# Optimization experiments

Hardware: AMD Instinct MI355X
Metric: run time of the kernel (lower is better)

Reference implementation:

```python
import jax, jax.numpy as jnp
import numpy as np

N = 16384; T = 65536; H = 128; G = 512; E = 65536; NEI = 32768
NIT = 4  # num_interactions
NL = 4   # finaldepth (hidden layers after the first)
EPS = 1e-5
INV = float(1.0 / np.sqrt(1.0 + EPS))  # fresh BatchNorm1d in eval mode: running_mean=0, running_var=1


def _bn(x, g, b):
    # eval-mode BatchNorm with mean=0, var=1: (x - 0)/sqrt(1+eps)*gamma + beta
    return x * (g * INV) + b


def setup_inputs() -> dict:
    key = jax.random.key(0)
    ks = jax.random.split(key, 16)
    inp = {}
    inp["node_positions"] = jax.random.normal(ks[0], (N, 2), jnp.float32)
    inp["edge_index_2rd"] = jax.random.randint(ks[1], (3, T), 0, N)  # (i, j, k) triplets
    inp["edx_jk"] = jax.random.randint(ks[2], (T,), 0, E)
    inp["edx_ij"] = jax.random.randint(ks[3], (T,), 0, E)
    inp["num_edge_inside"] = NEI
    inp["node_to_feature"] = jax.random.randint(ks[4], (N,), 0, G)
    # mlp_geo: Linear(3, H) + BN
    inp["Wg"] = jax.random.normal(ks[5], (3, H), jnp.float32) / np.sqrt(3.0)
    inp["bg"] = jnp.zeros((H,), jnp.float32)
    inp["gamg"] = 1.0 + 0.1 * jax.random.normal(ks[6], (H,), jnp.float32)
    inp["betg"] = 0.1 * jax.random.normal(ks[7], (H,), jnp.float32)
    # per-interaction (NIT), per-edge-type-group (4) MLPs
    inp["W0"] = jax.random.normal(ks[8], (NIT, 4, 4 * H, H), jnp.float32) / np.sqrt(4.0 * H)
    inp["b0"] = jnp.zeros((NIT, 4, H), jnp.float32)
    inp["g0"] = 1.0 + 0.1 * jax.random.normal(ks[9], (NIT, 4, H), jnp.float32)
    inp["be0"] = 0.1 * jax.random.normal(ks[10], (NIT, 4, H), jnp.float32)
    inp["Wh"] = jax.random.normal(ks[11], (NIT, NL, 4, H, H), jnp.float32) / np.sqrt(float(H))
    inp["bh"] = jnp.zeros((NIT, NL, 4, H), jnp.float32)
    inp["gh"] = 1.0 + 0.1 * jax.random.normal(ks[12], (NIT, NL, 4, H), jnp.float32)
    inp["beh"] = 0.1 * jax.random.normal(ks[13], (NIT, NL, 4, H), jnp.float32)
    inp["att"] = jnp.ones((4,), jnp.float32)
    return inp


def reference(node_positions, Wg, bg, gamg, betg, W0, b0, g0, be0, Wh, bh, gh, beh, att,
              edge_index_2rd, edx_jk, edx_ij, num_edge_inside, node_to_feature):
    i, j, k = edge_index_2rd[0], edge_index_2rd[1], edge_index_2rd[2]
    # geometric features of each triplet (i<-j<-k)
    v1 = node_positions[j] - node_positions[i]   # [T,2]
    v2 = node_positions[k] - node_positions[j]   # [T,2]
    d_ij = jnp.linalg.norm(v1, axis=1)
    d_jk = jnp.linalg.norm(v2, axis=1)
    cross = v1[:, 0] * v2[:, 1] - v1[:, 1] * v2[:, 0]
    dot = jnp.sum(v1 * v2, axis=1)
    theta = jnp.arctan2(jnp.abs(cross), dot)
    geo = jnp.stack([d_ij, d_jk, theta], axis=-1)        # [T,3]
    geo = jax.nn.relu(_bn(geo @ Wg + bg, gamg, betg))    # [T,H] geo_encoding

    # 4 mutually exclusive edge-type masks
    in1 = edx_ij < num_edge_inside
    in2 = edx_jk < num_edge_inside
    masks = jnp.stack([in1 & in2, in1 & ~in2, ~in1 & in2, ~in1 & ~in2], axis=0)  # [4,T]
    mask_f = masks.astype(geo.dtype)[:, :, None]         # [4,T,1]

    num_nodes = node_positions.shape[0]
    nf = jnp.zeros((num_nodes, H), geo.dtype)            # input_feature = zeros
    outs = []
    for it in range(NIT):
        x = jnp.concatenate([nf[i], nf[j], nf[k], geo], axis=-1)  # [T,4H]
        h = jnp.einsum('ti,gio->gto', x, W0[it]) + b0[it][:, None, :]
        h = jax.nn.relu(_bn(h, g0[it][:, None, :], be0[it][:, None, :]))
        for l in range(NL):
            h = jnp.einsum('gti,gio->gto', h, Wh[it, l]) + bh[it, l][:, None, :]
            h = jax.nn.relu(_bn(h, gh[it, l][:, None, :], beh[it, l][:, None, :]))
        h = jax.nn.leaky_relu(h, 0.01) * att[:, None, None]       # [4,T,H]
        x_out = jnp.sum(h * mask_f, axis=0)                       # disjoint masks -> select
        nf = jax.ops.segment_sum(x_out, i, num_segments=num_nodes)  # scatter_add over i
        outs.append(nf)
    out = jnp.concatenate(outs, axis=1)                           # [N, NIT*H]
    emb = jax.ops.segment_sum(out, node_to_feature, num_segments=G)  # global_add_pool
    return jnp.minimum(emb, 1.0e6)
```

## Files before the change

### kernel.cpp

```cpp
#include <hip/hip_runtime.h>
#include <hip/hip_bf16.h>
#include <math.h>

#define N_NODES 16384
#define T_TRI   65536
#define H_DIM   128
#define G_POOL  512
#define NITER   4
#define NLAY    4
#define RMAX    (T_TRI + 512)
#define MT64    (RMAX / 64)

#define INV_STD 0.9999950000374996f

typedef __attribute__((ext_vector_type(8))) short bhalf8;
typedef __attribute__((ext_vector_type(4))) float f32x4;

__device__ __forceinline__ unsigned short f2b(float f) {
    unsigned int u = __float_as_uint(f);
    unsigned int r = (u + 0x7fffu + ((u >> 16) & 1u)) >> 16;
    return (unsigned short)r;
}
__device__ __forceinline__ float b2f(unsigned short b) {
    return __uint_as_float(((unsigned int)b) << 16);
}


__device__ __forceinline__ int group_of(int eij, int ejk, int nei) {
    return ((eij < nei) ? 0 : 2) + ((ejk < nei) ? 0 : 1);
}

__global__ void histboth_k(const int* __restrict__ edxjk, const int* __restrict__ edxij,
                           const int* __restrict__ neip, const int* __restrict__ eidx,
                           int* __restrict__ ints, int* __restrict__ cnt) {
    __shared__ int lc[4];
    if (threadIdx.x < 4) lc[threadIdx.x] = 0;
    __syncthreads();
    int t = blockIdx.x * 256 + threadIdx.x;
    int nei = *neip;
    int g = group_of(edxij[t], edxjk[t], nei);
    atomicAdd(&lc[g], 1);
    atomicAdd(&cnt[eidx[t]], 1);
    __syncthreads();
    if (threadIdx.x < 4) atomicAdd(&ints[threadIdx.x], lc[threadIdx.x]);
}

__global__ void scanoff_k(int* __restrict__ ints, int* __restrict__ cnt,
                          int* __restrict__ row_start) {
    __shared__ int part[256];
    int tid = threadIdx.x;
    if (tid == 0) {
        int a = 0;
        ints[8] = 0;
        for (int g = 0; g < 4; ++g) {
            a = (a + ints[g] + 127) & ~127;
            ints[9 + g] = a;
        }
    }
    int base = tid * 64;
    int s = 0;
    for (int q = 0; q < 64; ++q) s += cnt[base + q];
    part[tid] = s;
    __syncthreads();
    if (tid == 0) {
        int run = 0;
        for (int q = 0; q < 256; ++q) { int v = part[q]; part[q] = run; run += v; }
        row_start[N_NODES] = run;
    }
    __syncthreads();
    int p = part[tid];
    for (int q = 0; q < 64; ++q) {
        int c = cnt[base + q];
        row_start[base + q] = p;
        cnt[base + q] = p;
        p += c;
    }
}

__global__ void scatboth_k(const int* __restrict__ edxjk, const int* __restrict__ edxij,
                           const int* __restrict__ neip, const int* __restrict__ eidx,
                           int* __restrict__ ints, int* __restrict__ rowmap,
                           int* __restrict__ cursor, int* __restrict__ row_ids) {
    int t = blockIdx.x * 256 + threadIdx.x;
    int nei = *neip;
    int g = group_of(edxij[t], edxjk[t], nei);
    int lane = threadIdx.x & 63;
    unsigned long long msame = 0;
    #pragma unroll
    for (int q = 0; q < 4; ++q) {
        unsigned long long mq = __ballot(g == q);
        if (g == q) msame = mq;
    }
    int leader = __ffsll((long long)msame) - 1;
    int rank = __popcll(msame & ((1ull << lane) - 1ull));
    int base = 0;
    if (lane == leader) base = atomicAdd(&ints[4 + g], __popcll(msame));
    base = __shfl(base, leader);
    int pos = ints[8 + g] + base + rank;
    rowmap[pos] = t;
    int slot = atomicAdd(&cursor[eidx[t]], 1);
    row_ids[slot] = pos;
}


__global__ void t0_k(const float* __restrict__ W0, unsigned short* __restrict__ WT0) {
    __shared__ float t[32][33];
    int b = blockIdx.x;
    int ig = b >> 6;
    int kt = (b >> 2) & 15;
    int nt = b & 3;
    int tx = threadIdx.x & 31, ty = threadIdx.x >> 5;
    const float* src = W0 + ((size_t)ig * 512 + kt * 32) * 128 + nt * 32;
    #pragma unroll
    for (int q = 0; q < 4; ++q) { int r = q * 8 + ty; t[r][tx] = src[(size_t)r * 128 + tx]; }
    __syncthreads();
    unsigned short* dst = WT0 + ((size_t)ig * 128 + nt * 32) * 512 + kt * 32;
    #pragma unroll
    for (int q = 0; q < 4; ++q) { int r = q * 8 + ty; dst[(size_t)r * 512 + tx] = f2b(t[tx][r]); }
}

__global__ void th_k(const float* __restrict__ Wh, unsigned short* __restrict__ WTh) {
    __shared__ float t[32][33];
    int b = blockIdx.x;
    int ilg = b >> 4;
    int kt = (b >> 2) & 3;
    int nt = b & 3;
    int tx = threadIdx.x & 31, ty = threadIdx.x >> 5;
    const float* src = Wh + ((size_t)ilg * 128 + kt * 32) * 128 + nt * 32;
    #pragma unroll
    for (int q = 0; q < 4; ++q) { int r = q * 8 + ty; t[r][tx] = src[(size_t)r * 128 + tx]; }
    __syncthreads();
    unsigned short* dst = WTh + ((size_t)ilg * 128 + nt * 32) * 128 + kt * 32;
    #pragma unroll
    for (int q = 0; q < 4; ++q) { int r = q * 8 + ty; dst[(size_t)r * 128 + tx] = f2b(t[tx][r]); }
}


__global__ void geo_k(const float* __restrict__ pos, const int* __restrict__ eidx,
                      const float* __restrict__ Wg, const float* __restrict__ bg,
                      const float* __restrict__ gamg, const float* __restrict__ betg,
                      unsigned short* __restrict__ geob) {
    int t = blockIdx.x * 16 + (threadIdx.x >> 4);
    int h0 = (threadIdx.x & 15) * 8;
    int ni = eidx[t], nj = eidx[T_TRI + t], nk = eidx[2 * T_TRI + t];
    float ix = pos[2 * ni], iy = pos[2 * ni + 1];
    float jx = pos[2 * nj], jy = pos[2 * nj + 1];
    float kx = pos[2 * nk], ky = pos[2 * nk + 1];
    float v1x = jx - ix, v1y = jy - iy;
    float v2x = kx - jx, v2y = ky - jy;
    float dij = sqrtf(v1x * v1x + v1y * v1y);
    float djk = sqrtf(v2x * v2x + v2y * v2y);
    float cr = v1x * v2y - v1y * v2x;
    float dt = v1x * v2x + v1y * v2y;
    float th = atan2f(fabsf(cr), dt);
    unsigned int ov[4];
    #pragma unroll
    for (int q = 0; q < 4; ++q) {
        unsigned int lo = 0, hi = 0;
        #pragma unroll
        for (int e = 0; e < 2; ++e) {
            int h = h0 + q * 2 + e;
            float v = dij * Wg[h] + djk * Wg[128 + h] + th * Wg[256 + h] + bg[h];
            v = v * (gamg[h] * INV_STD) + betg[h];
            v = fmaxf(v, 0.0f);
            if (e == 0) lo = f2b(v); else hi = f2b(v);
        }
        ov[q] = lo | (hi << 16);
    }
    int4 o = { (int)ov[0], (int)ov[1], (int)ov[2], (int)ov[3] };
    *reinterpret_cast<int4*>(&geob[(size_t)t * 128 + h0]) = o;
}


template<int SKIPNF>
__global__ __launch_bounds__(256, 4) void chain_k(
    const unsigned short* __restrict__ nfb, const unsigned short* __restrict__ geob,
    const int* __restrict__ eidx, const int* __restrict__ rowmap,
    const int* __restrict__ aoff, const unsigned short* __restrict__ WT0,
    const float* __restrict__ b0, const float* __restrict__ g0, const float* __restrict__ be0,
    const unsigned short* __restrict__ WTh,
    const float* __restrict__ bhp, const float* __restrict__ ghp, const float* __restrict__ behp,
    const float* __restrict__ att, unsigned short* __restrict__ hfinal,
    int it) {
    __shared__ unsigned short sh[64 * 128];
    __shared__ unsigned short sa[2][64 * 64];

    const int r0 = blockIdx.x * 64;
    int g = 0;
    if (r0 >= aoff[1]) g = 1;
    if (r0 >= aoff[2]) g = 2;
    if (r0 >= aoff[3]) g = 3;
    const int tid = threadIdx.x;
    const int lane = tid & 63;
    const int w = tid >> 6;
    const int lr = lane & 15, lq = lane >> 4;

    const int myrow = tid >> 3;
    const int mycolb = (tid & 7) * 8;
    int ttv[2], offi[2], offj[2], offk2[2], offt[2];
    #pragma unroll
    for (int p = 0; p < 2; ++p) {
        int row = p * 32 + myrow;
        int tt = rowmap[r0 + row];
        ttv[p] = tt;
        int ts = tt < 0 ? 0 : tt;
        offt[p] = ts * 128;
        if (!SKIPNF) {
            offi[p]  = eidx[ts] * 128;
            offj[p]  = eidx[T_TRI + ts] * 128;
            offk2[p] = eidx[2 * T_TRI + ts] * 128;
        }
    }

    f32x4 acc[4][2];
    const f32x4 zero4 = {0.f, 0.f, 0.f, 0.f};
    #pragma unroll
    for (int m = 0; m < 4; ++m)
        #pragma unroll
        for (int n = 0; n < 2; ++n) acc[m][n] = zero4;

    const unsigned short* Wt = WT0 + (size_t)(it * 4 + g) * 128 * 512;
    constexpr int KSTEPS = SKIPNF ? 2 : 8;
    constexpr int KBASE  = SKIPNF ? 384 : 0;
    int4 ra[2];

    {
        const int k0 = KBASE;
        const int region = k0 >> 7, half = k0 & 127;
        #pragma unroll
        for (int p = 0; p < 2; ++p) {
            int4 v = {0, 0, 0, 0};
            if (ttv[p] >= 0) {
                const unsigned short* src =
                    region == 0 ? nfb + offi[p] :
                    region == 1 ? nfb + offj[p] :
                    region == 2 ? nfb + offk2[p] :
                                  geob + offt[p];
                v = *reinterpret_cast<const int4*>(src + half + mycolb);
            }
            int row = p * 32 + myrow;
            *reinterpret_cast<int4*>(&sa[0][row * 64 + (((tid & 7) ^ (row & 7)) << 3)]) = v;
        }
        __syncthreads();
    }

    #pragma unroll
    for (int s = 0; s < KSTEPS; ++s) {
        const int cur = s & 1;
        const int k0 = KBASE + s * 64;
        if (s + 1 < KSTEPS) {
            const int k1 = k0 + 64;
            const int region = k1 >> 7, half = k1 & 127;
            #pragma unroll
            for (int p = 0; p < 2; ++p) {
                int4 v = {0, 0, 0, 0};
                if (ttv[p] >= 0) {
                    const unsigned short* src =
                        region == 0 ? nfb + offi[p] :
                        region == 1 ? nfb + offj[p] :
                        region == 2 ? nfb + offk2[p] :
                                      geob + offt[p];
                    v = *reinterpret_cast<const int4*>(src + half + mycolb);
                }
                ra[p] = v;
            }
        }
        bhalf8 rbf[2][2];
        #pragma unroll
        for (int n = 0; n < 2; ++n) {
            int nn = 32 * w + 16 * n + lr;
            #pragma unroll
            for (int ks = 0; ks < 2; ++ks)
                rbf[n][ks] = *reinterpret_cast<const bhalf8*>(Wt + (size_t)nn * 512 + k0 + ks * 32 + lq * 8);
        }
        #pragma unroll
        for (int ks = 0; ks < 2; ++ks) {
            bhalf8 af[4];
            #pragma unroll
            for (int m = 0; m < 4; ++m) {
                int row = 16 * m + lr;
                int c8 = (4 * ks + lq) ^ (row & 7);
                af[m] = *reinterpret_cast<const bhalf8*>(&sa[cur][row * 64 + (c8 << 3)]);
            }
            #pragma unroll
            for (int m = 0; m < 4; ++m)
                #pragma unroll
                for (int n = 0; n < 2; ++n)
                    acc[m][n] = __builtin_amdgcn_mfma_f32_16x16x32_bf16(af[m], rbf[n][ks], acc[m][n], 0, 0, 0);
        }
        if (s + 1 < KSTEPS) {
            #pragma unroll
            for (int p = 0; p < 2; ++p) {
                int row = p * 32 + myrow;
                *reinterpret_cast<int4*>(&sa[cur ^ 1][row * 64 + (((tid & 7) ^ (row & 7)) << 3)]) = ra[p];
            }
        }
        __syncthreads();
    }

    {
        const float* bb = b0 + (it * 4 + g) * 128;
        const float* gg = g0 + (it * 4 + g) * 128;
        const float* be = be0 + (it * 4 + g) * 128;
        #pragma unroll
        for (int n = 0; n < 2; ++n) {
            int col = 32 * w + 16 * n + lr;
            float sc = gg[col] * INV_STD;
            float bbc = bb[col], bec = be[col];
            int gc = col >> 3, cl = col & 7;
            #pragma unroll
            for (int m = 0; m < 4; ++m)
                #pragma unroll
                for (int r = 0; r < 4; ++r) {
                    int row = 16 * m + 4 * lq + r;
                    float v = fmaxf((acc[m][n][r] + bbc) * sc + bec, 0.0f);
                    sh[row * 128 + ((gc ^ (row & 7)) << 3) + cl] = f2b(v);
                }
        }
    }
    __syncthreads();

    for (int l = 0; l < NLAY; ++l) {
        const unsigned short* Wl = WTh + (size_t)((it * NLAY + l) * 4 + g) * 128 * 128;
        #pragma unroll
        for (int m = 0; m < 4; ++m)
            #pragma unroll
            for (int n = 0; n < 2; ++n) acc[m][n] = zero4;
        #pragma unroll
        for (int kk = 0; kk < 4; ++kk) {
            bhalf8 af[4], bf[2];
            #pragma unroll
            for (int n = 0; n < 2; ++n) {
                int nn = 32 * w + 16 * n + lr;
                bf[n] = *reinterpret_cast<const bhalf8*>(Wl + (size_t)nn * 128 + kk * 32 + lq * 8);
            }
            #pragma unroll
            for (int m = 0; m < 4; ++m) {
                int row = 16 * m + lr;
                int gc = (4 * kk + lq) ^ (row & 7);
                af[m] = *reinterpret_cast<const bhalf8*>(&sh[row * 128 + (gc << 3)]);
            }
            #pragma unroll
            for (int m = 0; m < 4; ++m)
                #pragma unroll
                for (int n = 0; n < 2; ++n)
                    acc[m][n] = __builtin_amdgcn_mfma_f32_16x16x32_bf16(af[m], bf[n], acc[m][n], 0, 0, 0);
        }
        __syncthreads();
        if (l + 1 < NLAY) {
            const int ilg = (it * NLAY + l) * 4 + g;
            const float* bb = bhp + (size_t)ilg * 128;
            const float* gg = ghp + (size_t)ilg * 128;
            const float* be = behp + (size_t)ilg * 128;
            #pragma unroll
            for (int n = 0; n < 2; ++n) {
                int col = 32 * w + 16 * n + lr;
                float sc = gg[col] * INV_STD;
                float bbc = bb[col], bec = be[col];
                int gc = col >> 3, cl = col & 7;
                #pragma unroll
                for (int m = 0; m < 4; ++m)
                    #pragma unroll
                    for (int r = 0; r < 4; ++r) {
                        int row = 16 * m + 4 * lq + r;
                        float v = fmaxf((acc[m][n][r] + bbc) * sc + bec, 0.0f);
                        sh[row * 128 + ((gc ^ (row & 7)) << 3) + cl] = f2b(v);
                    }
            }
            __syncthreads();
        }
    }

    {
        const int ilg = (it * NLAY + (NLAY - 1)) * 4 + g;
        const float* bb = bhp + (size_t)ilg * 128;
        const float* gg = ghp + (size_t)ilg * 128;
        const float* be = behp + (size_t)ilg * 128;
        float attg = att[g];
        #pragma unroll
        for (int n = 0; n < 2; ++n) {
            int col = 32 * w + 16 * n + lr;
            float sc = gg[col] * INV_STD;
            float bbc = bb[col], bec = be[col];
            int gc = col >> 3, cl = col & 7;
            #pragma unroll
            for (int m = 0; m < 4; ++m)
                #pragma unroll
                for (int r = 0; r < 4; ++r) {
                    int row = 16 * m + 4 * lq + r;
                    float v = fmaxf((acc[m][n][r] + bbc) * sc + bec, 0.0f) * attg;
                    sh[row * 128 + ((gc ^ (row & 7)) << 3) + cl] = f2b(v);
                }
        }
    }
    __syncthreads();
    #pragma unroll
    for (int p = 0; p < 4; ++p) {
        int idx = p * 256 + tid;
        int row = idx >> 4, gd = idx & 15;
        int4 v = *reinterpret_cast<const int4*>(&sh[row * 128 + ((gd ^ (row & 7)) << 3)]);
        *reinterpret_cast<int4*>(&hfinal[(size_t)(r0 + row) * 128 + gd * 8]) = v;
    }
}


__global__ void reduce_k(const unsigned short* __restrict__ hfinal,
                         const int* __restrict__ row_start, const int* __restrict__ row_ids,
                         const int* __restrict__ ntf, unsigned short* __restrict__ nfb,
                         float* __restrict__ emb, int itoff) {
    int n = blockIdx.x * 2 + (threadIdx.x >> 7);
    int c = threadIdx.x & 127;
    int s = row_start[n], e = row_start[n + 1];
    float acc = 0.0f;
    for (int r = s; r < e; ++r) {
        int rid = row_ids[r];
        acc += b2f(hfinal[(size_t)rid * 128 + c]);
    }
    nfb[(size_t)n * 128 + c] = f2b(acc);
    atomicAdd(&emb[(size_t)ntf[n] * 512 + itoff + c], acc);
}

__global__ void clamp_k(const float* __restrict__ emb, float* __restrict__ out) {
    int i = blockIdx.x * 256 + threadIdx.x;
    out[i] = fminf(emb[i], 1.0e6f);
}


extern "C" void kernel_launch(void* const* d_in, const int* in_sizes, int n_in,
                              void* d_out, int out_size, void* d_ws, size_t ws_size,
                              hipStream_t stream) {
    (void)in_sizes; (void)n_in; (void)out_size; (void)ws_size;
    const float* pos   = (const float*)d_in[0];
    const int*   eidx  = (const int*)d_in[1];
    const int*   edxjk = (const int*)d_in[2];
    const int*   edxij = (const int*)d_in[3];
    const int*   neip  = (const int*)d_in[4];
    const int*   ntf   = (const int*)d_in[5];
    const float* Wg    = (const float*)d_in[6];
    const float* bg    = (const float*)d_in[7];
    const float* gamg  = (const float*)d_in[8];
    const float* betg  = (const float*)d_in[9];
    const float* W0    = (const float*)d_in[10];
    const float* b0    = (const float*)d_in[11];
    const float* g0    = (const float*)d_in[12];
    const float* be0   = (const float*)d_in[13];
    const float* Wh    = (const float*)d_in[14];
    const float* bhp   = (const float*)d_in[15];
    const float* ghp   = (const float*)d_in[16];
    const float* behp  = (const float*)d_in[17];
    const float* att   = (const float*)d_in[18];

    char* w = (char*)d_ws;
    size_t off = 0;
    auto alloc = [&](size_t b) -> char* {
        char* p = w + off;
        off += (b + 255) & ~(size_t)255;
        return p;
    };
    int* ints            = (int*)alloc(256);
    int* rowmap          = (int*)alloc((size_t)RMAX * 4);
    int* cnt             = (int*)alloc((size_t)N_NODES * 4);
    int* row_start       = (int*)alloc((size_t)(N_NODES + 1) * 4);
    int* row_ids         = (int*)alloc((size_t)T_TRI * 4);
    unsigned short* WT0  = (unsigned short*)alloc((size_t)16 * 128 * 512 * 2);
    unsigned short* WTh  = (unsigned short*)alloc((size_t)64 * 128 * 128 * 2);
    unsigned short* geob = (unsigned short*)alloc((size_t)T_TRI * 128 * 2);
    unsigned short* nfb  = (unsigned short*)alloc((size_t)N_NODES * 128 * 2);
    unsigned short* hfin = (unsigned short*)alloc((size_t)RMAX * 128 * 2);
    float* emb           = (float*)alloc((size_t)G_POOL * 512 * 4);

    hipMemsetAsync(ints, 0, 256, stream);
    hipMemsetAsync(rowmap, 0xFF, (size_t)RMAX * 4, stream);
    hipMemsetAsync(cnt, 0, (size_t)N_NODES * 4, stream);
    hipMemsetAsync(emb, 0, (size_t)G_POOL * 512 * 4, stream);

    histboth_k<<<256, 256, 0, stream>>>(edxjk, edxij, neip, eidx, ints, cnt);
    scanoff_k<<<1, 256, 0, stream>>>(ints, cnt, row_start);
    scatboth_k<<<256, 256, 0, stream>>>(edxjk, edxij, neip, eidx, ints, rowmap, cnt, row_ids);
    t0_k<<<1024, 256, 0, stream>>>(W0, WT0);
    th_k<<<1024, 256, 0, stream>>>(Wh, WTh);
    geo_k<<<T_TRI / 16, 256, 0, stream>>>(pos, eidx, Wg, bg, gamg, betg, geob);

    for (int it = 0; it < NITER; ++it) {
        if (it == 0)
            chain_k<1><<<MT64, 256, 0, stream>>>(nfb, geob, eidx, rowmap, ints + 8, WT0, b0, g0, be0,
                                                 WTh, bhp, ghp, behp, att, hfin, it);
        else
            chain_k<0><<<MT64, 256, 0, stream>>>(nfb, geob, eidx, rowmap, ints + 8, WT0, b0, g0, be0,
                                                 WTh, bhp, ghp, behp, att, hfin, it);
        reduce_k<<<N_NODES / 2, 256, 0, stream>>>(hfin, row_start, row_ids, ntf, nfb, emb, it * 128);
    }

    clamp_k<<<1024, 256, 0, stream>>>(emb, (float*)d_out);
}
```

Measured before the change: 445.2 us.

## Restructure chain kernel to single-wave 32-row tiles with register-prefetched A

The MLP chain kernel moves from 256-thread blocks over 64 rows to one-wave blocks over 32 rows, each wave computing all 128 output columns. The first-layer A operand is gathered straight into registers with a 4-deep prefetch instead of being staged through double-buffered shared memory. The aim is to drop all __syncthreads and LDS staging while doubling the grid for occupancy. In exchange, each wave reloads the full weight matrices from global or cache for only 32 rows, and the larger accumulator set raises register pressure.

```diff
diff --git a/kernel.cpp b/kernel.cpp
--- a/kernel.cpp
+++ b/kernel.cpp
@@ -9,7 +9,7 @@
 #define NITER   4
 #define NLAY    4
 #define RMAX    (T_TRI + 512)
-#define MT64    (RMAX / 64)
+#define MT32    (RMAX / 32)
 
 #define INV_STD 0.9999950000374996f
 
@@ -173,7 +173,7 @@
 
 
 template<int SKIPNF>
-__global__ __launch_bounds__(256, 4) void chain_k(
+__global__ __launch_bounds__(64) void chain_k(
     const unsigned short* __restrict__ nfb, const unsigned short* __restrict__ geob,
     const int* __restrict__ eidx, const int* __restrict__ rowmap,
     const int* __restrict__ aoff, const unsigned short* __restrict__ WT0,
@@ -182,120 +182,78 @@
     const float* __restrict__ bhp, const float* __restrict__ ghp, const float* __restrict__ behp,
     const float* __restrict__ att, unsigned short* __restrict__ hfinal,
     int it) {
-    __shared__ unsigned short sh[64 * 128];
-    __shared__ unsigned short sa[2][64 * 64];
-
-    const int r0 = blockIdx.x * 64;
+    __shared__ unsigned short shw[32 * 128];
+
+    const int r0 = blockIdx.x * 32;
     int g = 0;
     if (r0 >= aoff[1]) g = 1;
     if (r0 >= aoff[2]) g = 2;
     if (r0 >= aoff[3]) g = 3;
-    const int tid = threadIdx.x;
-    const int lane = tid & 63;
-    const int w = tid >> 6;
+    const int lane = threadIdx.x & 63;
     const int lr = lane & 15, lq = lane >> 4;
 
-    const int myrow = tid >> 3;
-    const int mycolb = (tid & 7) * 8;
-    int ttv[2], offi[2], offj[2], offk2[2], offt[2];
-    #pragma unroll
-    for (int p = 0; p < 2; ++p) {
-        int row = p * 32 + myrow;
-        int tt = rowmap[r0 + row];
-        ttv[p] = tt;
+    int ttm[2];
+    const unsigned short* pi[2];
+    const unsigned short* pj[2];
+    const unsigned short* pk[2];
+    const unsigned short* pg[2];
+    #pragma unroll
+    for (int m = 0; m < 2; ++m) {
+        int tt = rowmap[r0 + 16 * m + lr];
+        ttm[m] = tt;
         int ts = tt < 0 ? 0 : tt;
-        offt[p] = ts * 128;
+        pg[m] = geob + (size_t)ts * 128;
         if (!SKIPNF) {
-            offi[p]  = eidx[ts] * 128;
-            offj[p]  = eidx[T_TRI + ts] * 128;
-            offk2[p] = eidx[2 * T_TRI + ts] * 128;
-        }
-    }
-
-    f32x4 acc[4][2];
+            pi[m] = nfb + (size_t)eidx[ts] * 128;
+            pj[m] = nfb + (size_t)eidx[T_TRI + ts] * 128;
+            pk[m] = nfb + (size_t)eidx[2 * T_TRI + ts] * 128;
+        } else {
+            pi[m] = pj[m] = pk[m] = pg[m];
+        }
+    }
+
+    f32x4 acc[2][8];
     const f32x4 zero4 = {0.f, 0.f, 0.f, 0.f};
     #pragma unroll
-    for (int m = 0; m < 4; ++m)
-        #pragma unroll
-        for (int n = 0; n < 2; ++n) acc[m][n] = zero4;
+    for (int m = 0; m < 2; ++m)
+        #pragma unroll
+        for (int n = 0; n < 8; ++n) acc[m][n] = zero4;
 
     const unsigned short* Wt = WT0 + (size_t)(it * 4 + g) * 128 * 512;
-    constexpr int KSTEPS = SKIPNF ? 2 : 8;
-    constexpr int KBASE  = SKIPNF ? 384 : 0;
-    int4 ra[2];
-
-    {
-        const int k0 = KBASE;
-        const int region = k0 >> 7, half = k0 & 127;
-        #pragma unroll
-        for (int p = 0; p < 2; ++p) {
-            int4 v = {0, 0, 0, 0};
-            if (ttv[p] >= 0) {
-                const unsigned short* src =
-                    region == 0 ? nfb + offi[p] :
-                    region == 1 ? nfb + offj[p] :
-                    region == 2 ? nfb + offk2[p] :
-                                  geob + offt[p];
-                v = *reinterpret_cast<const int4*>(src + half + mycolb);
-            }
-            int row = p * 32 + myrow;
-            *reinterpret_cast<int4*>(&sa[0][row * 64 + (((tid & 7) ^ (row & 7)) << 3)]) = v;
-        }
-        __syncthreads();
-    }
-
-    #pragma unroll
-    for (int s = 0; s < KSTEPS; ++s) {
-        const int cur = s & 1;
-        const int k0 = KBASE + s * 64;
-        if (s + 1 < KSTEPS) {
-            const int k1 = k0 + 64;
-            const int region = k1 >> 7, half = k1 & 127;
-            #pragma unroll
-            for (int p = 0; p < 2; ++p) {
-                int4 v = {0, 0, 0, 0};
-                if (ttv[p] >= 0) {
-                    const unsigned short* src =
-                        region == 0 ? nfb + offi[p] :
-                        region == 1 ? nfb + offj[p] :
-                        region == 2 ? nfb + offk2[p] :
-                                      geob + offt[p];
-                    v = *reinterpret_cast<const int4*>(src + half + mycolb);
-                }
-                ra[p] = v;
-            }
-        }
-        bhalf8 rbf[2][2];
-        #pragma unroll
-        for (int n = 0; n < 2; ++n) {
-            int nn = 32 * w + 16 * n + lr;
-            #pragma unroll
-            for (int ks = 0; ks < 2; ++ks)
-                rbf[n][ks] = *reinterpret_cast<const bhalf8*>(Wt + (size_t)nn * 512 + k0 + ks * 32 + lq * 8);
-        }
-        #pragma unroll
-        for (int ks = 0; ks < 2; ++ks) {
-            bhalf8 af[4];
-            #pragma unroll
-            for (int m = 0; m < 4; ++m) {
-                int row = 16 * m + lr;
-                int c8 = (4 * ks + lq) ^ (row & 7);
-                af[m] = *reinterpret_cast<const bhalf8*>(&sa[cur][row * 64 + (c8 << 3)]);
-            }
-            #pragma unroll
-            for (int m = 0; m < 4; ++m)
-                #pragma unroll
-                for (int n = 0; n < 2; ++n)
-                    acc[m][n] = __builtin_amdgcn_mfma_f32_16x16x32_bf16(af[m], rbf[n][ks], acc[m][n], 0, 0, 0);
-        }
-        if (s + 1 < KSTEPS) {
-            #pragma unroll
-            for (int p = 0; p < 2; ++p) {
-                int row = p * 32 + myrow;
-                *reinterpret_cast<int4*>(&sa[cur ^ 1][row * 64 + (((tid & 7) ^ (row & 7)) << 3)]) = ra[p];
-            }
-        }
-        __syncthreads();
+    constexpr int KS0 = SKIPNF ? 12 : 0;
+
+    auto loadA = [&](int ks, int m) -> int4 {
+        const int region = ks >> 2;
+        const int off = (ks & 3) * 32 + lq * 8;
+        const unsigned short* src =
+            region == 0 ? pi[m] : region == 1 ? pj[m] : region == 2 ? pk[m] : pg[m];
+        int4 v = {0, 0, 0, 0};
+        if (ttm[m] >= 0) v = *reinterpret_cast<const int4*>(src + off);
+        return v;
+    };
+
+    int4 pf[2][4];
+    #pragma unroll
+    for (int s = 0; s < 4; ++s) {
+        pf[0][s] = loadA(KS0 + s, 0);
+        pf[1][s] = loadA(KS0 + s, 1);
+    }
+    #pragma unroll
+    for (int ks = KS0; ks < 16; ++ks) {
+        const int slot = (ks - KS0) & 3;
+        bhalf8 a0 = *reinterpret_cast<bhalf8*>(&pf[0][slot]);
+        bhalf8 a1 = *reinterpret_cast<bhalf8*>(&pf[1][slot]);
+        if (ks + 4 < 16) {
+            pf[0][slot] = loadA(ks + 4, 0);
+            pf[1][slot] = loadA(ks + 4, 1);
+        }
+        #pragma unroll
+        for (int n = 0; n < 8; ++n) {
+            bhalf8 bf = *reinterpret_cast<const bhalf8*>(
+                Wt + (size_t)(16 * n + lr) * 512 + ks * 32 + lq * 8);
+            acc[0][n] = __builtin_amdgcn_mfma_f32_16x16x32_bf16(a0, bf, acc[0][n], 0, 0, 0);
+            acc[1][n] = __builtin_amdgcn_mfma_f32_16x16x32_bf16(a1, bf, acc[1][n], 0, 0, 0);
+        }
     }
 
     {
@@ -303,102 +261,73 @@
         const float* gg = g0 + (it * 4 + g) * 128;
         const float* be = be0 + (it * 4 + g) * 128;
         #pragma unroll
-        for (int n = 0; n < 2; ++n) {
-            int col = 32 * w + 16 * n + lr;
+        for (int n = 0; n < 8; ++n) {
+            int col = 16 * n + lr;
             float sc = gg[col] * INV_STD;
             float bbc = bb[col], bec = be[col];
             int gc = col >> 3, cl = col & 7;
             #pragma unroll
-            for (int m = 0; m < 4; ++m)
+            for (int m = 0; m < 2; ++m)
                 #pragma unroll
                 for (int r = 0; r < 4; ++r) {
                     int row = 16 * m + 4 * lq + r;
                     float v = fmaxf((acc[m][n][r] + bbc) * sc + bec, 0.0f);
-                    sh[row * 128 + ((gc ^ (row & 7)) << 3) + cl] = f2b(v);
+                    shw[row * 128 + ((gc ^ (row & 7)) << 3) + cl] = f2b(v);
                 }
         }
     }
-    __syncthreads();
 
     for (int l = 0; l < NLAY; ++l) {
         const unsigned short* Wl = WTh + (size_t)((it * NLAY + l) * 4 + g) * 128 * 128;
-        #pragma unroll
-        for (int m = 0; m < 4; ++m)
+        f32x4 hacc[2][8];
+        #pragma unroll
+        for (int m = 0; m < 2; ++m)
             #pragma unroll
-            for (int n = 0; n < 2; ++n) acc[m][n] = zero4;
+            for (int n = 0; n < 8; ++n) hacc[m][n] = zero4;
         #pragma unroll
         for (int kk = 0; kk < 4; ++kk) {
-            bhalf8 af[4], bf[2];
+            bhalf8 af[2];
             #pragma unroll
-            for (int n = 0; n < 2; ++n) {
-                int nn = 32 * w + 16 * n + lr;
-                bf[n] = *reinterpret_cast<const bhalf8*>(Wl + (size_t)nn * 128 + kk * 32 + lq * 8);
+            for (int m = 0; m < 2; ++m) {
+                int row = 16 * m + lr;
+                int gc = (4 * kk + lq) ^ (row & 7);
+                af[m] = *reinterpret_cast<const bhalf8*>(&shw[row * 128 + (gc << 3)]);
             }
             #pragma unroll
-            for (int m = 0; m < 4; ++m) {
-                int row = 16 * m + lr;
-                int gc = (4 * kk + lq) ^ (row & 7);
-                af[m] = *reinterpret_cast<const bhalf8*>(&sh[row * 128 + (gc << 3)]);
+            for (int n = 0; n < 8; ++n) {
+                bhalf8 bf = *reinterpret_cast<const bhalf8*>(
+                    Wl + (size_t)(16 * n + lr) * 128 + kk * 32 + lq * 8);
+                hacc[0][n] = __builtin_amdgcn_mfma_f32_16x16x32_bf16(af[0], bf, hacc[0][n], 0, 0, 0);
+                hacc[1][n] = __builtin_amdgcn_mfma_f32_16x16x32_bf16(af[1], bf, hacc[1][n], 0, 0, 0);
             }
-            #pragma unroll
-            for (int m = 0; m < 4; ++m)
-                #pragma unroll
-                for (int n = 0; n < 2; ++n)
-                    acc[m][n] = __builtin_amdgcn_mfma_f32_16x16x32_bf16(af[m], bf[n], acc[m][n], 0, 0, 0);
-        }
-        __syncthreads();
-        if (l + 1 < NLAY) {
-            const int ilg = (it * NLAY + l) * 4 + g;
-            const float* bb = bhp + (size_t)ilg * 128;
-            const float* gg = ghp + (size_t)ilg * 128;
-            const float* be = behp + (size_t)ilg * 128;
-            #pragma unroll
-            for (int n = 0; n < 2; ++n) {
-                int col = 32 * w + 16 * n + lr;
-                float sc = gg[col] * INV_STD;
-                float bbc = bb[col], bec = be[col];
-                int gc = col >> 3, cl = col & 7;
-                #pragma unroll
-                for (int m = 0; m < 4; ++m)
-                    #pragma unroll
-                    for (int r = 0; r < 4; ++r) {
-                        int row = 16 * m + 4 * lq + r;
-                        float v = fmaxf((acc[m][n][r] + bbc) * sc + bec, 0.0f);
-                        sh[row * 128 + ((gc ^ (row & 7)) << 3) + cl] = f2b(v);
-                    }
-            }
-            __syncthreads();
-        }
-    }
-
-    {
-        const int ilg = (it * NLAY + (NLAY - 1)) * 4 + g;
+        }
+        const int ilg = (it * NLAY + l) * 4 + g;
         const float* bb = bhp + (size_t)ilg * 128;
         const float* gg = ghp + (size_t)ilg * 128;
         const float* be = behp + (size_t)ilg * 128;
-        float attg = att[g];
-        #pragma unroll
-        for (int n = 0; n < 2; ++n) {
-            int col = 32 * w + 16 * n + lr;
+        float attg = (l == NLAY - 1) ? att[g] : 1.0f;
+        #pragma unroll
+        for (int n = 0; n < 8; ++n) {
+            int col = 16 * n + lr;
             float sc = gg[col] * INV_STD;
             float bbc = bb[col], bec = be[col];
             int gc = col >> 3, cl = col & 7;
             #pragma unroll
-            for (int m = 0; m < 4; ++m)
+            for (int m = 0; m < 2; ++m)
                 #pragma unroll
                 for (int r = 0; r < 4; ++r) {
                     int row = 16 * m + 4 * lq + r;
-                    float v = fmaxf((acc[m][n][r] + bbc) * sc + bec, 0.0f) * attg;
-                    sh[row * 128 + ((gc ^ (row & 7)) << 3) + cl] = f2b(v);
+                    float v = fmaxf((hacc[m][n][r] + bbc) * sc + bec, 0.0f) * attg;
+                    shw[row * 128 + ((gc ^ (row & 7)) << 3) + cl] = f2b(v);
                 }
         }
     }
-    __syncthreads();
-    #pragma unroll
-    for (int p = 0; p < 4; ++p) {
-        int idx = p * 256 + tid;
+
+    #pragma unroll
+    for (int p = 0; p < 8; ++p) {
+        int idx = p * 64 + lane;
         int row = idx >> 4, gd = idx & 15;
-        int4 v = *reinterpret_cast<const int4*>(&sh[row * 128 + ((gd ^ (row & 7)) << 3)]);
+        int4 v = *reinterpret_cast<const int4*>(&shw[row * 128 + ((gd ^ (row & 7)) << 3)]);
         *reinterpret_cast<int4*>(&hfinal[(size_t)(r0 + row) * 128 + gd * 8]) = v;
     }
 }
@@ -483,11 +412,11 @@
 
     for (int it = 0; it < NITER; ++it) {
         if (it == 0)
-            chain_k<1><<<MT64, 256, 0, stream>>>(nfb, geob, eidx, rowmap, ints + 8, WT0, b0, g0, be0,
-                                                 WTh, bhp, ghp, behp, att, hfin, it);
+            chain_k<1><<<MT32, 64, 0, stream>>>(nfb, geob, eidx, rowmap, ints + 8, WT0, b0, g0, be0,
+                                                WTh, bhp, ghp, behp, att, hfin, it);
         else
-            chain_k<0><<<MT64, 256, 0, stream>>>(nfb, geob, eidx, rowmap, ints + 8, WT0, b0, g0, be0,
-                                                 WTh, bhp, ghp, behp, att, hfin, it);
+            chain_k<0><<<MT32, 64, 0, stream>>>(nfb, geob, eidx, rowmap, ints + 8, WT0, b0, g0, be0,
+                                                WTh, bhp, ghp, behp, att, hfin, it);
         reduce_k<<<N_NODES / 2, 256, 0, stream>>>(hfin, row_start, row_ids, ntf, nfb, emb, it * 128);
     }
 
```

Result: slower. 692.0 us (+55.4%).

## Stage whole gathered A tile into LDS via global_load_lds upfront

Applied to the files above, without the earlier changes.

Replaces the register-staged, double-buffered gather of the first-layer A operand with direct global-to-LDS loads (global_load_lds) that fetch all K steps of the tile at once. The per-step syncs go away, leaving a single barrier before the MFMA loop. LDS grows to hold the full 64x512 tile and is shared with the hidden-layer buffer, and launch bounds drop from 4 to 2 blocks per CU. Padded rows (negative rowmap) are no longer zeroed; they read triplet 0 instead, which may change padded outputs.

```diff
diff --git a/kernel.cpp b/kernel.cpp
--- a/kernel.cpp
+++ b/kernel.cpp
@@ -15,6 +15,8 @@
 
 typedef __attribute__((ext_vector_type(8))) short bhalf8;
 typedef __attribute__((ext_vector_type(4))) float f32x4;
+typedef __attribute__((address_space(3))) void lds_t;
+typedef __attribute__((address_space(1))) const void gmem_t;
 
 __device__ __forceinline__ unsigned short f2b(float f) {
     unsigned int u = __float_as_uint(f);
@@ -173,7 +175,7 @@
 
 
 template<int SKIPNF>
-__global__ __launch_bounds__(256, 4) void chain_k(
+__global__ __launch_bounds__(256, 2) void chain_k(
     const unsigned short* __restrict__ nfb, const unsigned short* __restrict__ geob,
     const int* __restrict__ eidx, const int* __restrict__ rowmap,
     const int* __restrict__ aoff, const unsigned short* __restrict__ WT0,
@@ -182,8 +184,10 @@
     const float* __restrict__ bhp, const float* __restrict__ ghp, const float* __restrict__ behp,
     const float* __restrict__ att, unsigned short* __restrict__ hfinal,
     int it) {
-    __shared__ unsigned short sh[64 * 128];
-    __shared__ unsigned short sa[2][64 * 64];
+    constexpr int KSTEPS = SKIPNF ? 2 : 8;
+    constexpr int KS0    = SKIPNF ? 6 : 0;
+    __shared__ unsigned short sa[KSTEPS * 64 * 64];
+    unsigned short* sh = sa;
 
     const int r0 = blockIdx.x * 64;
     int g = 0;
@@ -195,20 +199,31 @@
     const int w = tid >> 6;
     const int lr = lane & 15, lq = lane >> 4;
 
-    const int myrow = tid >> 3;
-    const int mycolb = (tid & 7) * 8;
-    int ttv[2], offi[2], offj[2], offk2[2], offt[2];
-    #pragma unroll
-    for (int p = 0; p < 2; ++p) {
-        int row = p * 32 + myrow;
+    const int dcol = ((lane & 7) ^ (lane >> 3)) * 8;
+    const unsigned short* psrc[2][4];
+    #pragma unroll
+    for (int q = 0; q < 2; ++q) {
+        int row = w * 16 + q * 8 + (lane >> 3);
         int tt = rowmap[r0 + row];
-        ttv[p] = tt;
         int ts = tt < 0 ? 0 : tt;
-        offt[p] = ts * 128;
+        psrc[q][3] = geob + (size_t)ts * 128;
         if (!SKIPNF) {
-            offi[p]  = eidx[ts] * 128;
-            offj[p]  = eidx[T_TRI + ts] * 128;
-            offk2[p] = eidx[2 * T_TRI + ts] * 128;
+            psrc[q][0] = nfb + (size_t)eidx[ts] * 128;
+            psrc[q][1] = nfb + (size_t)eidx[T_TRI + ts] * 128;
+            psrc[q][2] = nfb + (size_t)eidx[2 * T_TRI + ts] * 128;
+        }
+    }
+
+    #pragma unroll
+    for (int s = 0; s < KSTEPS; ++s) {
+        const int ks = KS0 + s;
+        const int region = ks >> 1;
+        const int half = (ks & 1) * 64;
+        #pragma unroll
+        for (int q = 0; q < 2; ++q) {
+            const unsigned short* gsrc = psrc[q][region] + half + dcol;
+            unsigned short* ldst = &sa[(s * 64 + w * 16 + q * 8) * 64];
+            __builtin_amdgcn_global_load_lds((gmem_t*)gsrc, (lds_t*)ldst, 16, 0, 0);
         }
     }
 
@@ -219,84 +234,39 @@
         #pragma unroll
         for (int n = 0; n < 2; ++n) acc[m][n] = zero4;
 
+    __syncthreads();
+
     const unsigned short* Wt = WT0 + (size_t)(it * 4 + g) * 128 * 512;
-    constexpr int KSTEPS = SKIPNF ? 2 : 8;
-    constexpr int KBASE  = SKIPNF ? 384 : 0;
-    int4 ra[2];
-
-    {
-        const int k0 = KBASE;
-        const int region = k0 >> 7, half = k0 & 127;
-        #pragma unroll
-        for (int p = 0; p < 2; ++p) {
-            int4 v = {0, 0, 0, 0};
-            if (ttv[p] >= 0) {
-                const unsigned short* src =
-                    region == 0 ? nfb + offi[p] :
-                    region == 1 ? nfb + offj[p] :
-                    region == 2 ? nfb + offk2[p] :
-                                  geob + offt[p];
-                v = *reinterpret_cast<const int4*>(src + half + mycolb);
-            }
-            int row = p * 32 + myrow;
-            *reinterpret_cast<int4*>(&sa[0][row * 64 + (((tid & 7) ^ (row & 7)) << 3)]) = v;
-        }
-        __syncthreads();
-    }
-
     #pragma unroll
     for (int s = 0; s < KSTEPS; ++s) {
-        const int cur = s & 1;
-        const int k0 = KBASE + s * 64;
-        if (s + 1 < KSTEPS) {
-            const int k1 = k0 + 64;
-            const int region = k1 >> 7, half = k1 & 127;
-            #pragma unroll
-            for (int p = 0; p < 2; ++p) {
-                int4 v = {0, 0, 0, 0};
-                if (ttv[p] >= 0) {
-                    const unsigned short* src =
-                        region == 0 ? nfb + offi[p] :
-                        region == 1 ? nfb + offj[p] :
-                        region == 2 ? nfb + offk2[p] :
-                                      geob + offt[p];
-                    v = *reinterpret_cast<const int4*>(src + half + mycolb);
-                }
-                ra[p] = v;
-            }
-        }
+        const int kabs = (KS0 + s) * 64;
+        const unsigned short* As = &sa[s * 64 * 64];
         bhalf8 rbf[2][2];
         #pragma unroll
         for (int n = 0; n < 2; ++n) {
             int nn = 32 * w + 16 * n + lr;
             #pragma unroll
-            for (int ks = 0; ks < 2; ++ks)
-                rbf[n][ks] = *reinterpret_cast<const bhalf8*>(Wt + (size_t)nn * 512 + k0 + ks * 32 + lq * 8);
-        }
-        #pragma unroll
-        for (int ks = 0; ks < 2; ++ks) {
+            for (int ks2 = 0; ks2 < 2; ++ks2)
+                rbf[n][ks2] = *reinterpret_cast<const bhalf8*>(
+                    Wt + (size_t)nn * 512 + kabs + ks2 * 32 + lq * 8);
+        }
+        #pragma unroll
+        for (int ks2 = 0; ks2 < 2; ++ks2) {
             bhalf8 af[4];
             #pragma unroll
             for (int m = 0; m < 4; ++m) {
                 int row = 16 * m + lr;
-                int c8 = (4 * ks + lq) ^ (row & 7);
-                af[m] = *reinterpret_cast<const bhalf8*>(&sa[cur][row * 64 + (c8 << 3)]);
+                int c8 = (4 * ks2 + lq) ^ (row & 7);
+                af[m] = *reinterpret_cast<const bhalf8*>(&As[row * 64 + (c8 << 3)]);
             }
             #pragma unroll
             for (int m = 0; m < 4; ++m)
                 #pragma unroll
                 for (int n = 0; n < 2; ++n)
-                    acc[m][n] = __builtin_amdgcn_mfma_f32_16x16x32_bf16(af[m], rbf[n][ks], acc[m][n], 0, 0, 0);
-        }
-        if (s + 1 < KSTEPS) {
-            #pragma unroll
-            for (int p = 0; p < 2; ++p) {
-                int row = p * 32 + myrow;
-                *reinterpret_cast<int4*>(&sa[cur ^ 1][row * 64 + (((tid & 7) ^ (row & 7)) << 3)]) = ra[p];
-            }
-        }
-        __syncthreads();
-    }
+                    acc[m][n] = __builtin_amdgcn_mfma_f32_16x16x32_bf16(af[m], rbf[n][ks2], acc[m][n], 0, 0, 0);
+        }
+    }
+    __syncthreads();
 
     {
         const float* bb = b0 + (it * 4 + g) * 128;
```

New measurement: 468.6 us. 1.05x slower.
